# Optimization experiments

Measured on AMD Instinct MI355X. Metric: run time of the kernel, lower is better.

## Reference

```python
import jax, jax.numpy as jnp
import numpy as np

N, L, H, E, V, PAD = 128, 64, 512, 512, 32000, 0


def setup_inputs() -> dict:
    key = jax.random.key(0)
    ks = jax.random.split(key, 8)
    s_in = 1.0 / np.sqrt(E)
    s_sani = 1.0 / np.sqrt(2 * H)
    s_out = 1.0 / np.sqrt(H)
    labels = jax.random.randint(ks[0], (N, L), 0, V)
    emb_table = jax.random.normal(ks[1], (V, E), jnp.float32) * 0.02
    emb_table = emb_table.at[PAD].set(0.0)  # padding_idx row is zero-initialized
    W_in = jax.random.uniform(ks[2], (H, E), jnp.float32, -s_in, s_in)
    b_in = jax.random.uniform(ks[3], (H,), jnp.float32, -s_in, s_in)
    W_sani = jax.random.uniform(ks[4], (H, 2 * H), jnp.float32, -s_sani, s_sani)
    b_sani = jax.random.uniform(ks[5], (H,), jnp.float32, -s_sani, s_sani)
    W_out = jax.random.uniform(ks[6], (E, H), jnp.float32, -s_out, s_out)
    b_out = jax.random.uniform(ks[7], (E,), jnp.float32, -s_out, s_out)
    return dict(labels=labels, emb_table=emb_table, W_in=W_in, b_in=b_in,
                W_sani=W_sani, b_sani=b_sani, W_out=W_out, b_out=b_out)


def reference(labels, emb_table, W_in, b_in, W_sani, b_sani, W_out, b_out):
    n, l = labels.shape
    emb = emb_table[labels]                                   # [N,L,E]
    x = jnp.einsum('nle,he->nlh', emb, W_in) + b_in           # [N,L,H] input conversion
    h_dim = W_in.shape[0]

    def step(states, sc):
        s, h0 = sc                                            # h0: [N,H]
        def body(li, carry):
            h, st = carry
            prev = st[li]                                     # hiddenStateLast[li]
            new_h = jnp.concatenate([prev, h], axis=-1) @ W_sani.T + b_sani
            take = li < s                                     # triangular mask
            return (jnp.where(take, new_h, h),
                    st.at[li].set(jnp.where(take, h, prev)))
        h, states = jax.lax.fori_loop(0, l, body, (h0, states))
        states = states.at[s].set(h)                          # hiddenStateLast[s] = h
        return states, h                                      # outputStates[s] = h

    states0 = jnp.zeros((l, n, h_dim), x.dtype)
    _, outs = jax.lax.scan(step, states0, (jnp.arange(l), jnp.swapaxes(x, 0, 1)))
    # torch: pt.concat(outputStates, dim=0) -> [L*N, H], outputLayer, reshape(N,L,E)
    y = outs.reshape(l * n, h_dim) @ W_out.T + b_out
    y = y.reshape(n, l, E)  # faithful to the original (sequence-major) reshape
    # CrossEntropyLoss with float (probability) targets: classes along dim 1 (L)
    logp = jax.nn.log_softmax(y, axis=1)
    loss = -(emb * logp).sum(axis=1).mean()
    return loss
```

## Files before the change

kernel.cpp:

```cpp
#include <hip/hip_runtime.h>
#include <hip/hip_bf16.h>

typedef __attribute__((ext_vector_type(8))) short short8;
typedef __attribute__((ext_vector_type(4))) float floatx4;

#define NB 128
#define LS 64
#define HD 512
#define ED 512
#define NH 65536
#define LDA 72
#define LDC 136
#define LDCF 132

#define OFF_WIN    0ull
#define OFF_WOUT   524288ull
#define OFF_XT     1048576ull
#define OFF_LVL0   9437184ull
#define OFF_LVL1   17825792ull
#define OFF_OUTS   26214400ull
#define OFF_PHA    34603008ull
#define OFF_PLA    37224448ull
#define OFF_PHB    39845888ull
#define OFF_PLB    42467328ull
#define OFF_BCAT   45088768ull
#define OFF_BETA   52428800ull
#define OFF_PART   52436992ull
#define OFF_WSLO   52437504ull
#define OFF_Y      OFF_LVL0

static __device__ __forceinline__ unsigned short f2b(float f) {
  unsigned u = __float_as_uint(f);
  u += 0x7fffu + ((u >> 16) & 1u);
  return (unsigned short)(u >> 16);
}
static __device__ __forceinline__ float b2f(unsigned short h) {
  return __uint_as_float(((unsigned)h) << 16);
}

static __device__ __forceinline__ void gl_lds16(const unsigned short* g, unsigned short* l) {
  __builtin_amdgcn_global_load_lds(
      (const __attribute__((address_space(1))) void*)g,
      (__attribute__((address_space(3))) void*)l, 16, 0, 0);
}

static __device__ __forceinline__ uint4 cvt8hi(const float* s) {
  floatx4 f0 = *(const floatx4*)s;
  floatx4 f1 = *(const floatx4*)(s + 4);
  float f[8] = {f0.x, f0.y, f0.z, f0.w, f1.x, f1.y, f1.z, f1.w};
  unsigned short b[8];
#pragma unroll
  for (int k = 0; k < 8; ++k) b[k] = f2b(f[k]);
  uint4 u;
  u.x = b[0] | ((unsigned)b[1] << 16); u.y = b[2] | ((unsigned)b[3] << 16);
  u.z = b[4] | ((unsigned)b[5] << 16); u.w = b[6] | ((unsigned)b[7] << 16);
  return u;
}

__device__ __forceinline__ void gemm_core24(const unsigned short* As, const unsigned short* Bs,
                                            floatx4 acc[2][4], int wm, int wn, int lane) {
  const int rb = lane & 15;
  const int kg = (lane >> 4) * 8;
#pragma unroll
  for (int kk = 0; kk < 64; kk += 32) {
    short8 a[2], b[4];
#pragma unroll
    for (int i = 0; i < 2; ++i)
      a[i] = *(const short8*)&As[(wm * 32 + i * 16 + rb) * LDA + kk + kg];
#pragma unroll
    for (int j = 0; j < 4; ++j)
      b[j] = *(const short8*)&Bs[(wn * 64 + j * 16 + rb) * LDA + kk + kg];
#pragma unroll
    for (int i = 0; i < 2; ++i)
#pragma unroll
      for (int j = 0; j < 4; ++j)
        acc[i][j] = __builtin_amdgcn_mfma_f32_16x16x32_bf16(a[i], b[j], acc[i][j], 0, 0, 0);
  }
}

__device__ __forceinline__ void gemm_core64s(const unsigned short* As, const unsigned short* Bs,
                                             floatx4 acc[2][4], int wm, int wn, int lane) {
  const int rb = lane & 15;
  const int kg = (lane >> 4) * 8;
  const int xv = (rb & 7) * 8;
#pragma unroll
  for (int kk = 0; kk < 64; kk += 32) {
    const int co = (kk + kg) ^ xv;
    short8 a[2], b[4];
#pragma unroll
    for (int i = 0; i < 2; ++i)
      a[i] = *(const short8*)&As[(wm * 32 + i * 16 + rb) * 64 + co];
#pragma unroll
    for (int j = 0; j < 4; ++j)
      b[j] = *(const short8*)&Bs[(wn * 64 + j * 16 + rb) * 64 + co];
#pragma unroll
    for (int i = 0; i < 2; ++i)
#pragma unroll
      for (int j = 0; j < 4; ++j)
        acc[i][j] = __builtin_amdgcn_mfma_f32_16x16x32_bf16(a[i], b[j], acc[i][j], 0, 0, 0);
  }
}

__device__ __forceinline__ void stageA_emb(unsigned short* As, const float* table,
                                           const int* labels, int m0, int k0, int tid) {
  int r = tid >> 3, kc = (tid & 7) * 8;
#pragma unroll
  for (int p = 0; p < 2; ++p) {
    int row = r + p * 32;
    const float* s = table + (size_t)labels[m0 + row] * ED + k0 + kc;
    *(uint4*)&As[row * LDA + kc] = cvt8hi(s);
  }
}

__device__ __forceinline__ void stageB(unsigned short* Bs, const unsigned short* src, int ldB, int tid) {
  int r = tid >> 3, kc = (tid & 7) * 8;
#pragma unroll
  for (int p = 0; p < 4; ++p)
    *(uint4*)&Bs[(r + p * 32) * LDA + kc] = *(const uint4*)(src + (size_t)(r + p * 32) * ldB + kc);
}

__global__ __launch_bounds__(256) void k_gemm_emb(const float* __restrict__ table,
                                                  const int* __restrict__ labels,
                                                  const unsigned short* __restrict__ Wb,
                                                  const float* __restrict__ bias,
                                                  unsigned short* __restrict__ xt) {
  __shared__ unsigned short As[64 * LDA];
  __shared__ unsigned short Bs[128 * LDA];
  int tid = threadIdx.x;
  int mtile = blockIdx.x >> 2, ntile = blockIdx.x & 3;
  int m0 = mtile * 64, n0 = ntile * 128;
  int lane = tid & 63, wave = tid >> 6, wm = wave >> 1, wn = wave & 1;
  floatx4 acc[2][4] = {};
  for (int k0 = 0; k0 < 512; k0 += 64) {
    stageA_emb(As, table, labels, m0, k0, tid);
    stageB(Bs, Wb + (size_t)n0 * 512 + k0, 512, tid);
    __syncthreads();
    gemm_core24(As, Bs, acc, wm, wn, lane);
    __syncthreads();
  }
  int rb = lane & 15, rg = (lane >> 4) * 4;
#pragma unroll
  for (int i = 0; i < 2; ++i)
#pragma unroll
    for (int j = 0; j < 4; ++j) {
      int col = n0 + wn * 64 + j * 16 + rb;
      float bv = bias[col];
#pragma unroll
      for (int reg = 0; reg < 4; ++reg) {
        int m = m0 + wm * 32 + i * 16 + rg + reg;
        int n = m >> 6, l = m & 63;
        xt[((size_t)l * NB + n) * HD + col] = f2b(acc[i][j][reg] + bv);
      }
    }
}

__global__ __launch_bounds__(256) void k_cvtw(const float* __restrict__ Win,
                                              const float* __restrict__ Wsani,
                                              const float* __restrict__ Wout,
                                              unsigned short* __restrict__ dWin,
                                              unsigned short* __restrict__ dBcat1,
                                              unsigned short* __restrict__ dWsLo,
                                              unsigned short* __restrict__ dWout) {
  int i = blockIdx.x * 256 + threadIdx.x;
  if (i < 65536 || i >= 196608) {
    const float* src = (i < 65536) ? Win : Wout;
    unsigned short* dst = (i < 65536) ? dWin : dWout;
    int off = (i < 65536) ? i : i - 196608;
    floatx4 v = *(const floatx4*)(src + (size_t)off * 4);
    uint2 u;
    u.x = (unsigned)f2b(v.x) | ((unsigned)f2b(v.y) << 16);
    u.y = (unsigned)f2b(v.z) | ((unsigned)f2b(v.w) << 16);
    *(uint2*)(dst + (size_t)off * 4) = u;
  } else {
    int off = i - 65536;
    floatx4 v = *(const floatx4*)(Wsani + (size_t)off * 4);
    float f[4] = {v.x, v.y, v.z, v.w};
    unsigned short hb[4], lb[4];
#pragma unroll
    for (int k = 0; k < 4; ++k) {
      hb[k] = f2b(f[k]);
      lb[k] = f2b(f[k] - b2f(hb[k]));
    }
    uint2 h, l;
    h.x = hb[0] | ((unsigned)hb[1] << 16); h.y = hb[2] | ((unsigned)hb[3] << 16);
    l.x = lb[0] | ((unsigned)lb[1] << 16); l.y = lb[2] | ((unsigned)lb[3] << 16);
    *(uint2*)(dBcat1 + (size_t)off * 4) = h;
    *(uint2*)(dWsLo + (size_t)off * 4) = l;
  }
}

__global__ __launch_bounds__(256) void k_trW(const float* __restrict__ Ws,
                                             unsigned short* __restrict__ Phi,
                                             unsigned short* __restrict__ Plo) {
  __shared__ float t[64][65];
  int mat = blockIdx.x >> 6, tile = blockIdx.x & 63;
  int a0 = (tile >> 3) * 64, b0 = (tile & 7) * 64;
  int coloff = (mat == 0) ? 512 : 0;
  for (int pp = 0; pp < 16; ++pp) {
    int idx = pp * 256 + threadIdx.x, rr = idx >> 6, cc = idx & 63;
    t[rr][cc] = Ws[(size_t)(b0 + rr) * 1024 + coloff + a0 + cc];
  }
  __syncthreads();
  for (int pp = 0; pp < 16; ++pp) {
    int idx = pp * 256 + threadIdx.x, rr = idx >> 6, cc = idx & 63;
    float f = t[cc][rr];
    unsigned short hi = f2b(f);
    size_t o = (size_t)mat * 262144 + (size_t)(a0 + rr) * 512 + b0 + cc;
    Phi[o] = hi;
    Plo[o] = f2b(f - b2f(hi));
  }
}

__global__ __launch_bounds__(256) void k_coef(const unsigned short* __restrict__ Phi,
                                              const unsigned short* __restrict__ Plo,
                                              unsigned short* __restrict__ PhiOut,
                                              unsigned short* __restrict__ PloOut,
                                              const unsigned short* __restrict__ WsHi,
                                              const unsigned short* __restrict__ WsLo,
                                              int m) {
  __shared__ unsigned short lds[24576];
  unsigned short* const A0 = lds;
  unsigned short* const A1 = lds + 4096;
  unsigned short* const B0 = lds + 8192;
  unsigned short* const B1 = lds + 16384;
  const int tid = threadIdx.x;
  const int j = blockIdx.x >> 5, tile = blockIdx.x & 31;
  const int k0r = (tile >> 2) * 64, n0 = (tile & 3) * 128;
  const int lane = tid & 63, wave = tid >> 6, wm = wave >> 1, wn = wave & 1;
  const int rr_ = tid >> 3;
  const int kcs = (((tid & 7) ^ ((tid >> 3) & 7))) * 8;
  const int t_first = (j <= m) ? 0 : 1;
  const int nterms = ((j <= m) ? 1 : 0) + ((j >= 1) ? 1 : 0);
  const int nsteps = nterms * 24;

  floatx4 acc[2][4] = {};

#define STAGE_C(Ab, Bb, u)                                                           \
  { int term_ = t_first + (((u) >= 24) ? 1 : 0);                                     \
    int v_ = ((u) >> 3) % 3;                                                         \
    int t0_ = ((u) & 7) * 64;                                                        \
    const unsigned short* As_ = ((v_ == 2) ? Plo : Phi)                              \
        + (size_t)(term_ ? (j - 1) : j) * 262144 + (size_t)k0r * 512 + t0_;          \
    const unsigned short* Bs_ = ((v_ == 1) ? WsLo : WsHi)                            \
        + (size_t)n0 * 1024 + (term_ ? 0 : 512) + t0_;                               \
    unsigned short* lA = (Ab) + (tid >> 6) * 512;                                    \
    unsigned short* lB = (Bb) + (tid >> 6) * 512;                                    \
    gl_lds16(As_ + (size_t)rr_ * 512 + kcs, lA);                                     \
    gl_lds16(As_ + (size_t)(rr_ + 32) * 512 + kcs, lA + 2048);                       \
    gl_lds16(Bs_ + (size_t)rr_ * 1024 + kcs, lB);                                    \
    gl_lds16(Bs_ + (size_t)(rr_ + 32) * 1024 + kcs, lB + 2048);                      \
    gl_lds16(Bs_ + (size_t)(rr_ + 64) * 1024 + kcs, lB + 4096);                      \
    gl_lds16(Bs_ + (size_t)(rr_ + 96) * 1024 + kcs, lB + 6144); }

  STAGE_C(A0, B0, 0)
  __syncthreads();
  for (int u = 0; u < nsteps; u += 2) {
    if (u + 1 < nsteps) STAGE_C(A1, B1, u + 1)
    gemm_core64s(A0, B0, acc, wm, wn, lane);
    __syncthreads();
    if (u + 2 < nsteps) STAGE_C(A0, B0, u + 2)
    gemm_core64s(A1, B1, acc, wm, wn, lane);
    __syncthreads();
  }
#undef STAGE_C

  const int rb = lane & 15, rg = (lane >> 4) * 4;
#pragma unroll
  for (int i = 0; i < 2; ++i)
#pragma unroll
    for (int jj = 0; jj < 4; ++jj) {
      int col = n0 + wn * 64 + jj * 16 + rb;
#pragma unroll
      for (int reg = 0; reg < 4; ++reg) {
        int row = wm * 32 + i * 16 + rg + reg;
        float f = acc[i][jj][reg];
        unsigned short hi = f2b(f);
        size_t o = (size_t)j * 262144 + (size_t)(k0r + row) * 512 + col;
        PhiOut[o] = hi;
        PloOut[o] = f2b(f - b2f(hi));
      }
    }
}

__global__ __launch_bounds__(256) void k_trB(const unsigned short* __restrict__ Phi,
                                             unsigned short* __restrict__ Bout,
                                             int r) {
  __shared__ unsigned short t[64][68];
  int q = blockIdx.x >> 6, tile = blockIdx.x & 63;
  int t0 = (tile >> 3) * 64, i0 = (tile & 7) * 64;
  const unsigned short* P = Phi + (size_t)(r - q) * 262144;
  int ldB = (r + 1) * 512;
  for (int pp = 0; pp < 16; ++pp) {
    int idx = pp * 256 + threadIdx.x, rr = idx >> 6, cc = idx & 63;
    t[rr][cc] = P[(size_t)(t0 + rr) * 512 + i0 + cc];
  }
  __syncthreads();
  for (int pp = 0; pp < 16; ++pp) {
    int idx = pp * 256 + threadIdx.x, rr = idx >> 6, cc = idx & 63;
    Bout[(size_t)(i0 + rr) * ldB + q * 512 + t0 + cc] = t[cc][rr];
  }
}

__global__ __launch_bounds__(64) void k_bias_step(const float* __restrict__ Ws,
                                                  const float* __restrict__ b,
                                                  const float* __restrict__ bprev,
                                                  float* __restrict__ bout) {
  int i = blockIdx.x, t = threadIdx.x;
  float p = 0.f;
  for (int k = t; k < 512; k += 64)
    p += (Ws[(size_t)i * 1024 + k] + Ws[(size_t)i * 1024 + 512 + k]) * bprev[k];
#pragma unroll
  for (int off = 32; off > 0; off >>= 1) p += __shfl_down(p, off, 64);
  if (t == 0) bout[i] = p + b[i];
}

__global__ __launch_bounds__(256) void k_step(const unsigned short* __restrict__ src,
                                              unsigned short* __restrict__ dst,
                                              unsigned short* __restrict__ outs,
                                              const unsigned short* __restrict__ Bcat,
                                              const float* __restrict__ beta,
                                              int L_prev, int m, int nmain, int g) {
  __shared__ unsigned short lds[24576];
  unsigned short* const A0 = lds;
  unsigned short* const A1 = lds + 4096;
  unsigned short* const B0 = lds + 8192;
  unsigned short* const B1 = lds + 16384;
  const int tid = threadIdx.x, bid = blockIdx.x;
  const int mainWG = 32 * g;
  int r, s, nb0, n0;
  if (bid < mainWG) {
    const int xcd = bid & 7, w = bid >> 3;
    const int sgrp = xcd >> 1, ngrp = xcd & 1;
    const int s_rel = sgrp * g + (w >> 2);
    if (s_rel >= nmain) return;
    const int sub2 = w & 3;
    nb0 = (sub2 >> 1) * 64;
    n0 = (ngrp * 2 + (sub2 & 1)) * 128;
    r = m; s = L_prev + m + s_rel;
  } else {
    const int db = bid - mainWG;
    r = 1 + (db >> 3);
    const int sub = db & 7;
    nb0 = (sub >> 2) * 64; n0 = (sub & 3) * 128;
    s = L_prev + r;
  }
  const int ldB = (r + 1) * 512;
  const unsigned short* Bp = Bcat + (size_t)262144 * (((r - 1) * (r + 2)) >> 1);
  const unsigned short* abase = src + (size_t)(s - r) * NH + (size_t)nb0 * HD;
  const float* bet = beta + (size_t)(r - 1) * 512;
  const int nk = (r + 1) * 8;
  const int lane = tid & 63, wave = tid >> 6, wm = wave >> 1, wn = wave & 1;
  const int rr_ = tid >> 3;
  const int kcs = (((tid & 7) ^ ((tid >> 3) & 7))) * 8;

  floatx4 acc[2][4] = {};

#define STAGE(Ab, Bb, kcol)                                                          \
  { int q_ = (kcol) >> 9, ac_ = (kcol) & 511;                                        \
    const unsigned short* a0_ = abase + (size_t)q_ * NH + ac_;                       \
    unsigned short* lA = (Ab) + (tid >> 6) * 512;                                    \
    unsigned short* lB = (Bb) + (tid >> 6) * 512;                                    \
    gl_lds16(a0_ + (size_t)rr_ * HD + kcs, lA);                                      \
    gl_lds16(a0_ + (size_t)(rr_ + 32) * HD + kcs, lA + 2048);                        \
    gl_lds16(Bp + (size_t)(n0 + rr_) * ldB + (kcol) + kcs, lB);                      \
    gl_lds16(Bp + (size_t)(n0 + rr_ + 32) * ldB + (kcol) + kcs, lB + 2048);          \
    gl_lds16(Bp + (size_t)(n0 + rr_ + 64) * ldB + (kcol) + kcs, lB + 4096);          \
    gl_lds16(Bp + (size_t)(n0 + rr_ + 96) * ldB + (kcol) + kcs, lB + 6144); }

  STAGE(A0, B0, 0)
  __syncthreads();
  for (int k = 0; k < nk; k += 2) {
    if (k + 1 < nk) STAGE(A1, B1, (k + 1) * 64)
    gemm_core64s(A0, B0, acc, wm, wn, lane);
    __syncthreads();
    if (k + 2 < nk) STAGE(A0, B0, (k + 2) * 64)
    gemm_core64s(A1, B1, acc, wm, wn, lane);
    __syncthreads();
  }
#undef STAGE

  unsigned short* Ct = lds;
  const int rbc = lane & 15, rg = (lane >> 4) * 4;
#pragma unroll
  for (int i = 0; i < 2; ++i)
#pragma unroll
    for (int j = 0; j < 4; ++j) {
      int col = wn * 64 + j * 16 + rbc;
      float bv = bet[n0 + col];
#pragma unroll
      for (int reg = 0; reg < 4; ++reg) {
        int row = wm * 32 + i * 16 + rg + reg;
        Ct[row * LDC + col] = f2b(acc[i][j][reg] + bv);
      }
    }
  __syncthreads();
  const bool wdst = (r == m);
  const bool wout = (r < m) || (s == L_prev + m);
  unsigned short* d1 = dst  + (size_t)s * NH + (size_t)nb0 * HD + n0;
  unsigned short* d2 = outs + (size_t)s * NH + (size_t)nb0 * HD + n0;
  const int lrow = tid >> 4, lcol = (tid & 15) * 8;
#pragma unroll
  for (int sweep = 0; sweep < 4; ++sweep) {
    int row = sweep * 16 + lrow;
    uint4 v = *(const uint4*)&Ct[row * LDC + lcol];
    if (wdst) *(uint4*)(d1 + (size_t)row * HD + lcol) = v;
    if (wout) *(uint4*)(d2 + (size_t)row * HD + lcol) = v;
  }
}

__global__ __launch_bounds__(256) void k_gemm_out(const unsigned short* __restrict__ outs,
                                                  const unsigned short* __restrict__ Wb,
                                                  const float* __restrict__ bias,
                                                  float* __restrict__ Y) {
  __shared__ unsigned short lds[24576];
  unsigned short* const A0 = lds;
  unsigned short* const A1 = lds + 4096;
  unsigned short* const B0 = lds + 8192;
  unsigned short* const B1 = lds + 16384;
  const int tid = threadIdx.x;
  const int mtile = blockIdx.x >> 2, ntile = blockIdx.x & 3;
  const int m0 = mtile * 64, n0 = ntile * 128;
  const int lane = tid & 63, wave = tid >> 6, wm = wave >> 1, wn = wave & 1;
  const int rr_ = tid >> 3;
  const int kcs = (((tid & 7) ^ ((tid >> 3) & 7))) * 8;
  const unsigned short* abase = outs + (size_t)m0 * 512;
  const unsigned short* Bp = Wb + (size_t)n0 * 512;

  floatx4 acc[2][4] = {};

#define STAGE_O(Ab, Bb, kcol)                                                        \
  { unsigned short* lA = (Ab) + (tid >> 6) * 512;                                    \
    unsigned short* lB = (Bb) + (tid >> 6) * 512;                                    \
    gl_lds16(abase + (size_t)rr_ * 512 + (kcol) + kcs, lA);                          \
    gl_lds16(abase + (size_t)(rr_ + 32) * 512 + (kcol) + kcs, lA + 2048);            \
    gl_lds16(Bp + (size_t)rr_ * 512 + (kcol) + kcs, lB);                             \
    gl_lds16(Bp + (size_t)(rr_ + 32) * 512 + (kcol) + kcs, lB + 2048);               \
    gl_lds16(Bp + (size_t)(rr_ + 64) * 512 + (kcol) + kcs, lB + 4096);               \
    gl_lds16(Bp + (size_t)(rr_ + 96) * 512 + (kcol) + kcs, lB + 6144); }

  STAGE_O(A0, B0, 0)
  __syncthreads();
  for (int k = 0; k < 8; k += 2) {
    if (k + 1 < 8) STAGE_O(A1, B1, (k + 1) * 64)
    gemm_core64s(A0, B0, acc, wm, wn, lane);
    __syncthreads();
    if (k + 2 < 8) STAGE_O(A0, B0, (k + 2) * 64)
    gemm_core64s(A1, B1, acc, wm, wn, lane);
    __syncthreads();
  }
#undef STAGE_O

  float* Ctf = (float*)lds;
  const int rbc = lane & 15, rg = (lane >> 4) * 4;
#pragma unroll
  for (int i = 0; i < 2; ++i)
#pragma unroll
    for (int j = 0; j < 4; ++j) {
      int col = wn * 64 + j * 16 + rbc;
      float bv = bias[n0 + col];
#pragma unroll
      for (int reg = 0; reg < 4; ++reg) {
        int row = wm * 32 + i * 16 + rg + reg;
        Ctf[row * LDCF + col] = acc[i][j][reg] + bv;
      }
    }
  __syncthreads();
  const int lrow = tid >> 5, lc = (tid & 31) * 4;
#pragma unroll
  for (int sweep = 0; sweep < 8; ++sweep) {
    int row = sweep * 8 + lrow;
    uint4 v = *(const uint4*)&Ctf[row * LDCF + lc];
    *(uint4*)&Y[(size_t)(m0 + row) * 512 + n0 + lc] = v;
  }
}

__global__ void k_copy(const uint4* __restrict__ src, uint4* __restrict__ dst, int n) {
  int i = blockIdx.x * blockDim.x + threadIdx.x;
  if (i < n) dst[i] = src[i];
}

__global__ __launch_bounds__(256) void k_loss(const float* __restrict__ Y,
                                              const float* __restrict__ table,
                                              const int* __restrict__ labels,
                                              float* __restrict__ partials) {
  int n = blockIdx.x, tid = threadIdx.x;
  float total = 0.f;
#pragma unroll
  for (int e2 = 0; e2 < 2; ++e2) {
    int e = e2 * 256 + tid;
    float mx = -1e30f;
    for (int l = 0; l < 64; ++l)
      mx = fmaxf(mx, Y[(size_t)(n * 64 + l) * 512 + e]);
    float se = 0.f;
    for (int l = 0; l < 64; ++l)
      se += expf(Y[(size_t)(n * 64 + l) * 512 + e] - mx);
    float lse = mx + logf(se);
    for (int l = 0; l < 64; ++l) {
      float embv = table[(size_t)labels[n * 64 + l] * ED + e];
      total += embv * (Y[(size_t)(n * 64 + l) * 512 + e] - lse);
    }
  }
  __shared__ float red[256];
  red[tid] = total;
  __syncthreads();
  for (int s2 = 128; s2 > 0; s2 >>= 1) {
    if (tid < s2) red[tid] += red[tid + s2];
    __syncthreads();
  }
  if (tid == 0) partials[n] = red[0];
}

__global__ void k_final(const float* __restrict__ partials, float* __restrict__ out) {
  if (threadIdx.x == 0) {
    double s = 0.0;
    for (int i = 0; i < 128; ++i) s += (double)partials[i];
    out[0] = (float)(-s / 65536.0);
  }
}

extern "C" void kernel_launch(void* const* d_in, const int* in_sizes, int n_in,
                              void* d_out, int out_size, void* d_ws, size_t ws_size,
                              hipStream_t stream) {
  const int*   labels = (const int*)d_in[0];
  const float* table  = (const float*)d_in[1];
  const float* W_in   = (const float*)d_in[2];
  const float* b_in   = (const float*)d_in[3];
  const float* W_sani = (const float*)d_in[4];
  const float* b_sani = (const float*)d_in[5];
  const float* W_out  = (const float*)d_in[6];
  const float* b_out  = (const float*)d_in[7];

  char* ws = (char*)d_ws;
  unsigned short* Win_b  = (unsigned short*)(ws + OFF_WIN);
  unsigned short* Wout_b = (unsigned short*)(ws + OFF_WOUT);
  unsigned short* xt     = (unsigned short*)(ws + OFF_XT);
  unsigned short* lvl0   = (unsigned short*)(ws + OFF_LVL0);
  unsigned short* lvl1   = (unsigned short*)(ws + OFF_LVL1);
  unsigned short* outs   = (unsigned short*)(ws + OFF_OUTS);
  unsigned short* PhiA   = (unsigned short*)(ws + OFF_PHA);
  unsigned short* PloA   = (unsigned short*)(ws + OFF_PLA);
  unsigned short* PhiB   = (unsigned short*)(ws + OFF_PHB);
  unsigned short* PloB   = (unsigned short*)(ws + OFF_PLB);
  unsigned short* Bcat   = (unsigned short*)(ws + OFF_BCAT);
  float*          beta   = (float*)(ws + OFF_BETA);
  float*          parts  = (float*)(ws + OFF_PART);
  unsigned short* WsLo   = (unsigned short*)(ws + OFF_WSLO);
  float*          Y      = (float*)(ws + OFF_Y);

  k_cvtw<<<1024, 256, 0, stream>>>(W_in, W_sani, W_out, Win_b, Bcat, WsLo, Wout_b);
  k_gemm_emb<<<512, 256, 0, stream>>>(table, labels, Win_b, b_in, xt);
  k_copy<<<32, 256, 0, stream>>>((const uint4*)xt, (uint4*)outs, 8192);

  k_copy<<<1, 128, 0, stream>>>((const uint4*)b_sani, (uint4*)beta, 128);
  k_bias_step<<<512, 64, 0, stream>>>(W_sani, b_sani, beta,        beta + 512);
  k_bias_step<<<512, 64, 0, stream>>>(W_sani, b_sani, beta + 512,  beta + 1024);
  k_bias_step<<<512, 64, 0, stream>>>(W_sani, b_sani, beta + 1024, beta + 1536);

  k_trW <<<128, 256, 0, stream>>>(W_sani, PhiA, PloA);
  k_coef<<< 96, 256, 0, stream>>>(PhiA, PloA, PhiB, PloB, Bcat, WsLo, 1);
  k_trB <<<192, 256, 0, stream>>>(PhiB, Bcat + 524288, 2);
  k_coef<<<128, 256, 0, stream>>>(PhiB, PloB, PhiA, PloA, Bcat, WsLo, 2);
  k_trB <<<256, 256, 0, stream>>>(PhiA, Bcat + 1310720, 3);
  k_coef<<<160, 256, 0, stream>>>(PhiA, PloA, PhiB, PloB, Bcat, WsLo, 3);
  k_trB <<<320, 256, 0, stream>>>(PhiB, Bcat + 2359296, 4);

  const unsigned short* srcp = xt;
  for (int j = 1; j <= 16; ++j) {
    int L_prev = 4 * (j - 1);
    int m = (j == 16) ? 3 : 4;
    int nmain = 64 - (L_prev + m);
    int g = (nmain + 3) >> 2;
    unsigned short* dstp = ((j - 1) & 1) ? lvl1 : lvl0;
    k_step<<<32 * g + (m - 1) * 8, 256, 0, stream>>>(srcp, dstp, outs, Bcat, beta,
                                                     L_prev, m, nmain, g);
    srcp = dstp;
  }

  k_gemm_out<<<512, 256, 0, stream>>>(outs, Wout_b, b_out, Y);
  k_loss<<<128, 256, 0, stream>>>(Y, table, labels, parts);
  k_final<<<1, 64, 0, stream>>>(parts, (float*)d_out);
}
```

Baseline: 586.1 us.

## Fuse seven recurrence steps per launch instead of four, precomputing higher-order coefficients

Raises the number of recurrence steps collapsed into each k_step launch from 4 to 7. This cuts the sequential chain from 16 launches to 9. To do this, the precompute chain of bias steps and coefficient matrices is extended to order 7, and workspace offsets are moved so the larger coefficient buffers fit. The cost is more precompute work and larger matrix products per launch, plus more bf16 hi/lo rounding error accumulating in the higher-order coefficients.

```diff
diff --git a/kernel.cpp b/kernel.cpp
--- a/kernel.cpp
+++ b/kernel.cpp
@@ -12,6 +12,7 @@
 #define LDA 72
 #define LDC 136
 #define LDCF 132
+#define MSTEP 7
 
 #define OFF_WIN    0ull
 #define OFF_WOUT   524288ull
@@ -19,14 +20,14 @@
 #define OFF_LVL0   9437184ull
 #define OFF_LVL1   17825792ull
 #define OFF_OUTS   26214400ull
-#define OFF_PHA    34603008ull
-#define OFF_PLA    37224448ull
-#define OFF_PHB    39845888ull
-#define OFF_PLB    42467328ull
-#define OFF_BCAT   45088768ull
-#define OFF_BETA   52428800ull
-#define OFF_PART   52436992ull
-#define OFF_WSLO   52437504ull
+#define OFF_PHA    9437184ull
+#define OFF_PLA    13631488ull
+#define OFF_PHB    17825792ull
+#define OFF_PLB    22020096ull
+#define OFF_BCAT   34603008ull
+#define OFF_BETA   52953088ull
+#define OFF_PART   52967424ull
+#define OFF_WSLO   52969472ull
 #define OFF_Y      OFF_LVL0
 
 static __device__ __forceinline__ unsigned short f2b(float f) {
@@ -552,27 +553,30 @@
   k_copy<<<32, 256, 0, stream>>>((const uint4*)xt, (uint4*)outs, 8192);
 
   k_copy<<<1, 128, 0, stream>>>((const uint4*)b_sani, (uint4*)beta, 128);
-  k_bias_step<<<512, 64, 0, stream>>>(W_sani, b_sani, beta,        beta + 512);
-  k_bias_step<<<512, 64, 0, stream>>>(W_sani, b_sani, beta + 512,  beta + 1024);
-  k_bias_step<<<512, 64, 0, stream>>>(W_sani, b_sani, beta + 1024, beta + 1536);
-
-  k_trW <<<128, 256, 0, stream>>>(W_sani, PhiA, PloA);
-  k_coef<<< 96, 256, 0, stream>>>(PhiA, PloA, PhiB, PloB, Bcat, WsLo, 1);
-  k_trB <<<192, 256, 0, stream>>>(PhiB, Bcat + 524288, 2);
-  k_coef<<<128, 256, 0, stream>>>(PhiB, PloB, PhiA, PloA, Bcat, WsLo, 2);
-  k_trB <<<256, 256, 0, stream>>>(PhiA, Bcat + 1310720, 3);
-  k_coef<<<160, 256, 0, stream>>>(PhiA, PloA, PhiB, PloB, Bcat, WsLo, 3);
-  k_trB <<<320, 256, 0, stream>>>(PhiB, Bcat + 2359296, 4);
+  for (int r = 1; r < MSTEP; ++r)
+    k_bias_step<<<512, 64, 0, stream>>>(W_sani, b_sani, beta + (r - 1) * 512,
+                                        beta + r * 512);
+
+  k_trW<<<128, 256, 0, stream>>>(W_sani, PhiA, PloA);
+  for (int r = 1; r < MSTEP; ++r) {
+    unsigned short* sh = (r & 1) ? PhiA : PhiB;
+    unsigned short* sl = (r & 1) ? PloA : PloB;
+    unsigned short* dh = (r & 1) ? PhiB : PhiA;
+    unsigned short* dl = (r & 1) ? PloB : PloA;
+    k_coef<<<(r + 2) * 32, 256, 0, stream>>>(sh, sl, dh, dl, Bcat, WsLo, r);
+    int rr = r + 1;
+    size_t boff = (size_t)262144 * (((rr - 1) * (rr + 2)) >> 1);
+    k_trB<<<rr * 64 + 64, 256, 0, stream>>>(dh, Bcat + boff, rr);
+  }
 
   const unsigned short* srcp = xt;
-  for (int j = 1; j <= 16; ++j) {
-    int L_prev = 4 * (j - 1);
-    int m = (j == 16) ? 3 : 4;
-    int nmain = 64 - (L_prev + m);
+  for (int j = 1; j <= 9; ++j) {
+    int L_prev = MSTEP * (j - 1);
+    int nmain = 64 - (L_prev + MSTEP);
     int g = (nmain + 3) >> 2;
     unsigned short* dstp = ((j - 1) & 1) ? lvl1 : lvl0;
-    k_step<<<32 * g + (m - 1) * 8, 256, 0, stream>>>(srcp, dstp, outs, Bcat, beta,
-                                                     L_prev, m, nmain, g);
+    k_step<<<32 * g + (MSTEP - 1) * 8, 256, 0, stream>>>(srcp, dstp, outs, Bcat, beta,
+                                                         L_prev, MSTEP, nmain, g);
     srcp = dstp;
   }
 
```

Result: slower. 643.4 us (+9.8%).
